# Kernel optimization log

Measured on AMD Instinct MI355X. Metric: run time of the kernel, lower is better.

The kernel has to match this reference:

```python
import jax, jax.numpy as jnp
import numpy as np

EPS = 0.07      # sinkhorn temperature
ITERS = 7       # sinkhorn iterations
TINY = 1e-8
NORM_EPS = 1e-12  # F.normalize default clamp


def setup_inputs() -> dict:
    key = jax.random.key(0)
    k1, k2 = jax.random.split(key)
    x = jax.random.normal(k1, (64, 2048, 24, 12), dtype=jnp.float32)
    anchors = jax.random.normal(k2, (2, 2048), dtype=jnp.float32) * 0.02
    return {"x": x, "anchors": anchors}


def reference(x, anchors):
    B, C, H, W = x.shape
    HW = H * W
    # tokens: (B, HW, C)
    X = x.reshape(B, C, HW).transpose(0, 2, 1)
    Xn = X / jnp.maximum(jnp.linalg.norm(X, axis=-1, keepdims=True), NORM_EPS)
    An = anchors / jnp.maximum(jnp.linalg.norm(anchors, axis=-1, keepdims=True), NORM_EPS)
    # cosine cost (B, HW, 2)
    Cmat = 1.0 - jnp.einsum('bhc,kc->bhk', Xn, An)
    Kmat = jnp.exp(-Cmat / max(EPS, TINY)) + TINY
    a = jnp.full((B, HW), 1.0 / HW, dtype=Kmat.dtype)
    b = jnp.full((B, 2), 0.5, dtype=Kmat.dtype)

    def step(carry, _):
        u, v = carry
        Kv = jnp.einsum('bhk,bk->bh', Kmat, v) + TINY
        u = a / Kv
        KTu = jnp.einsum('bhk,bh->bk', Kmat, u) + TINY
        v = b / KTu
        return (u, v), None

    u0 = jnp.ones((B, HW), dtype=Kmat.dtype)
    v0 = jnp.ones((B, 2), dtype=Kmat.dtype)
    (u, v), _ = jax.lax.scan(step, (u0, v0), None, length=ITERS)
    # transport plan and soft masks
    P = Kmat * u[:, :, None] * v[:, None, :]          # (B, HW, 2)
    m = (P * HW).transpose(0, 2, 1).reshape(B, 2, H, W)
    # masked pooling for both prototypes at once
    num = jnp.einsum('bchw,bkhw->bkc', x, m)           # (B, 2, C)
    den = m.sum(axis=(2, 3)) + 1e-6                    # (B, 2)
    c = num / den[:, :, None]
    c0_vec = c[:, 0][:, :, None, None]                 # (B, C, 1, 1)
    c1_vec = c[:, 1][:, :, None, None]
    return (c0_vec, c1_vec, m)
```

## Files before the change

### kernel.cpp

```cpp
#include <hip/hip_runtime.h>

#define B_    64
#define C_    2048
#define HW_   288
#define EPS_  0.07f
#define TINY_ 1e-8f

__device__ __forceinline__ void acc3(const float4 v, float a0, float a1,
                                     float* ssq, float* sd0, float* sd1) {
  ssq[0] += v.x * v.x; ssq[1] += v.y * v.y; ssq[2] += v.z * v.z; ssq[3] += v.w * v.w;
  sd0[0] += v.x * a0;  sd0[1] += v.y * a0;  sd0[2] += v.z * a0;  sd0[3] += v.w * a0;
  sd1[0] += v.x * a1;  sd1[1] += v.y * a1;  sd1[2] += v.z * a1;  sd1[3] += v.w * a1;
}

__global__ __launch_bounds__(256) void k1_partials(
    const float* __restrict__ x, const float* __restrict__ anchors,
    float* __restrict__ part, int nch, int cpc) {
  int bi = blockIdx.x;
  int nblk = nch >> 2;
  int b  = bi / nblk;
  int cg = bi - b * nblk;
  int t = threadIdx.x, lane = t & 63, wid = t >> 6;
  int ch = cg * 4 + wid;
  int c0 = ch * cpc;
  const float* xb = x + ((size_t)b * C_ + c0) * HW_;
  bool tail = lane < 8;

  float ssq[4] = {0,0,0,0}, sd0[4] = {0,0,0,0}, sd1[4] = {0,0,0,0};
  float tsq[4] = {0,0,0,0}, td0[4] = {0,0,0,0}, td1[4] = {0,0,0,0};

#pragma unroll 4
  for (int r = 0; r < cpc; ++r) {
    const float4* xr = (const float4*)(xb + (size_t)r * HW_);
    float a0 = anchors[c0 + r];
    float a1 = anchors[C_ + c0 + r];
    float4 xa = xr[lane];
    acc3(xa, a0, a1, ssq, sd0, sd1);
    if (tail) {
      float4 xc = xr[64 + lane];
      acc3(xc, a0, a1, tsq, td0, td1);
    }
  }

  size_t PS = (size_t)B_ * nch * HW_;
  float* base = part + (size_t)(b * nch + ch) * HW_;
  float4* p0 = (float4*)base;
  float4* p1 = (float4*)(base + PS);
  float4* p2 = (float4*)(base + 2 * PS);
  p0[lane] = make_float4(ssq[0], ssq[1], ssq[2], ssq[3]);
  p1[lane] = make_float4(sd0[0], sd0[1], sd0[2], sd0[3]);
  p2[lane] = make_float4(sd1[0], sd1[1], sd1[2], sd1[3]);
  if (tail) {
    p0[64 + lane] = make_float4(tsq[0], tsq[1], tsq[2], tsq[3]);
    p1[64 + lane] = make_float4(td0[0], td0[1], td0[2], td0[3]);
    p2[64 + lane] = make_float4(td1[0], td1[1], td1[2], td1[3]);
  }
}

__global__ __launch_bounds__(256) void k1b_reduce(
    const float* __restrict__ part, float* __restrict__ red, int nch) {
  int idx = blockIdx.x * 256 + threadIdx.x;
  int plane = idx / (B_ * HW_);
  int rem = idx - plane * (B_ * HW_);
  int b = rem / HW_;
  int h = rem - b * HW_;
  const float* p = part + (size_t)plane * B_ * nch * HW_ + (size_t)b * nch * HW_ + h;
  float s = 0.f;
#pragma unroll 8
  for (int ch = 0; ch < nch; ++ch) s += p[(size_t)ch * HW_];
  red[idx] = s;
}

__device__ __forceinline__ void block_reduce2(
    float& p0, float& p1, volatile float* red0, volatile float* red1,
    int t, int nw) {
  int lane = t & 63, wid = t >> 6;
#pragma unroll
  for (int off = 32; off >= 1; off >>= 1) {
    p0 += __shfl_down(p0, off);
    p1 += __shfl_down(p1, off);
  }
  __syncthreads();
  if (lane == 0) { red0[wid] = p0; red1[wid] = p1; }
  __syncthreads();
  float s0 = 0.f, s1 = 0.f;
  for (int w = 0; w < nw; ++w) { s0 += red0[w]; s1 += red1[w]; }
  p0 = s0; p1 = s1;
}

__global__ __launch_bounds__(320) void k2_sinkhorn(
    const float* __restrict__ red, const float* __restrict__ anchors,
    float* __restrict__ out_m, float* __restrict__ invden) {
  int b = blockIdx.x, t = threadIdx.x;
  __shared__ float red0[8], red1[8];
  const int nw = 5;

  float a0 = 0.f, a1 = 0.f;
  for (int c = t; c < C_; c += 320) {
    float q0 = anchors[c], q1 = anchors[C_ + c];
    a0 += q0 * q0; a1 += q1 * q1;
  }
  block_reduce2(a0, a1, red0, red1, t, nw);
  float ian0 = 1.0f / fmaxf(sqrtf(a0), 1e-12f);
  float ian1 = 1.0f / fmaxf(sqrtf(a1), 1e-12f);

  float K0 = 0.f, K1 = 0.f;
  if (t < HW_) {
    float ssq = red[b * HW_ + t];
    float d0  = red[B_ * HW_ + b * HW_ + t];
    float d1  = red[2 * B_ * HW_ + b * HW_ + t];
    float ixn = 1.0f / fmaxf(sqrtf(ssq), 1e-12f);
    float cos0 = d0 * ixn * ian0;
    float cos1 = d1 * ixn * ian1;
    K0 = expf((cos0 - 1.0f) / EPS_) + TINY_;
    K1 = expf((cos1 - 1.0f) / EPS_) + TINY_;
  }

  float v0 = 1.f, v1 = 1.f, u = 0.f;
  for (int it = 0; it < 7; ++it) {
    if (t < HW_) u = (1.0f / (float)HW_) / (K0 * v0 + K1 * v1 + TINY_);
    float p0 = K0 * u, p1 = K1 * u;
    block_reduce2(p0, p1, red0, red1, t, nw);
    v0 = 0.5f / (p0 + TINY_);
    v1 = 0.5f / (p1 + TINY_);
  }

  float m0 = 0.f, m1 = 0.f;
  if (t < HW_) {
    m0 = K0 * u * v0 * (float)HW_;
    m1 = K1 * u * v1 * (float)HW_;
  }
  float q0 = m0, q1 = m1;
  block_reduce2(q0, q1, red0, red1, t, nw);
  if (t < HW_) {
    out_m[(b * 2 + 0) * HW_ + t] = m0;
    out_m[(b * 2 + 1) * HW_ + t] = m1;
  }
  if (t == 0) {
    invden[b * 2 + 0] = 1.0f / (q0 + 1e-6f);
    invden[b * 2 + 1] = 1.0f / (q1 + 1e-6f);
  }
}

__global__ __launch_bounds__(256) void k3_pool(
    const float* __restrict__ x, const float* __restrict__ m,
    const float* __restrict__ invden, float* __restrict__ out) {
  int bi = blockIdx.x;
  int b = bi >> 4, seg = bi & 15;
  int t = threadIdx.x;
  int lr = t >> 1, half = t & 1;
  int c = seg * 128 + lr;

  __shared__ float4 sm0[72], sm1[72];
  __shared__ float sinv[2];
  if (t < 72)       sm0[t]      = ((const float4*)(m + (b * 2 + 0) * HW_))[t];
  else if (t < 144) sm1[t - 72] = ((const float4*)(m + (b * 2 + 1) * HW_))[t - 72];
  if (t == 0) { sinv[0] = invden[2 * b]; sinv[1] = invden[2 * b + 1]; }
  __syncthreads();

  const float4* xr = (const float4*)(x + ((size_t)b * C_ + c) * HW_) + half * 36;
  const float4* w0p = sm0 + half * 36;
  const float4* w1p = sm1 + half * 36;
  float acc0 = 0.f, acc1 = 0.f;
#pragma unroll 4
  for (int i = 0; i < 36; ++i) {
    float4 xa = xr[i];
    float4 w0 = w0p[i];
    float4 w1 = w1p[i];
    acc0 += xa.x * w0.x + xa.y * w0.y + xa.z * w0.z + xa.w * w0.w;
    acc1 += xa.x * w1.x + xa.y * w1.y + xa.z * w1.z + xa.w * w1.w;
  }
  acc0 += __shfl_down(acc0, 1);
  acc1 += __shfl_down(acc1, 1);
  if (half == 0) {
    out[(size_t)b * C_ + c] = acc0 * sinv[0];
    out[(size_t)B_ * C_ + (size_t)b * C_ + c] = acc1 * sinv[1];
  }
}

extern "C" void kernel_launch(void* const* d_in, const int* in_sizes, int n_in,
                              void* d_out, int out_size, void* d_ws, size_t ws_size,
                              hipStream_t stream) {
  const float* x       = (const float*)d_in[0];
  const float* anchors = (const float*)d_in[1];
  float* out = (float*)d_out;

  float* invden = (float*)d_ws;
  float* red = invden + 128;
  float* part = red + 3 * B_ * HW_;
  int nch = 128;
  while (nch > 4 &&
         (size_t)(128 + 3 * B_ * HW_ + 3 * B_ * nch * HW_) * sizeof(float) > ws_size)
    nch >>= 1;
  int cpc = C_ / nch;

  float* out_m = out + 2 * B_ * C_;

  k1_partials<<<B_ * (nch / 4), 256, 0, stream>>>(x, anchors, part, nch, cpc);
  k1b_reduce<<<(3 * B_ * HW_) / 256, 256, 0, stream>>>(part, red, nch);
  k2_sinkhorn<<<B_, 320, 0, stream>>>(red, anchors, out_m, invden);
  k3_pool<<<B_ * 16, 256, 0, stream>>>(x, out_m, invden, out);
}
```

Before: 266.2 us.

## Restructure pooling kernel with register-held masks and fewer k1 channel splits

The pooling kernel now has 8 threads cooperate on each channel row, each reading a contiguous 9-float4 slice. Each thread keeps its mask weights in registers instead of shared memory, and each block loops over 256 channels. This gives coalesced row reads and removes the shared-memory staging and barrier, at the cost of 72 extra registers per thread and fewer blocks. Separately, the k1 channel split drops from 128 to 32, which shrinks the partial-sum buffer and the reduce pass. The trade-off is less parallelism in the first pass over x.

```diff
diff --git a/kernel.cpp b/kernel.cpp
--- a/kernel.cpp
+++ b/kernel.cpp
@@ -146,35 +146,40 @@
     const float* __restrict__ x, const float* __restrict__ m,
     const float* __restrict__ invden, float* __restrict__ out) {
   int bi = blockIdx.x;
-  int b = bi >> 4, seg = bi & 15;
-  int t = threadIdx.x;
-  int lr = t >> 1, half = t & 1;
-  int c = seg * 128 + lr;
-
-  __shared__ float4 sm0[72], sm1[72];
-  __shared__ float sinv[2];
-  if (t < 72)       sm0[t]      = ((const float4*)(m + (b * 2 + 0) * HW_))[t];
-  else if (t < 144) sm1[t - 72] = ((const float4*)(m + (b * 2 + 1) * HW_))[t - 72];
-  if (t == 0) { sinv[0] = invden[2 * b]; sinv[1] = invden[2 * b + 1]; }
-  __syncthreads();
-
-  const float4* xr = (const float4*)(x + ((size_t)b * C_ + c) * HW_) + half * 36;
-  const float4* w0p = sm0 + half * 36;
-  const float4* w1p = sm1 + half * 36;
-  float acc0 = 0.f, acc1 = 0.f;
-#pragma unroll 4
-  for (int i = 0; i < 36; ++i) {
-    float4 xa = xr[i];
-    float4 w0 = w0p[i];
-    float4 w1 = w1p[i];
-    acc0 += xa.x * w0.x + xa.y * w0.y + xa.z * w0.z + xa.w * w0.w;
-    acc1 += xa.x * w1.x + xa.y * w1.y + xa.z * w1.z + xa.w * w1.w;
-  }
-  acc0 += __shfl_down(acc0, 1);
-  acc1 += __shfl_down(acc1, 1);
-  if (half == 0) {
-    out[(size_t)b * C_ + c] = acc0 * sinv[0];
-    out[(size_t)B_ * C_ + (size_t)b * C_ + c] = acc1 * sinv[1];
+  int b = bi >> 3, seg = bi & 7;
+  int t = threadIdx.x, oct = t & 7, rl = t >> 3;
+
+  const float4* m0 = (const float4*)(m + (b * 2 + 0) * HW_);
+  const float4* m1 = (const float4*)(m + (b * 2 + 1) * HW_);
+  float4 w0[9], w1[9];
+#pragma unroll
+  for (int j = 0; j < 9; ++j) {
+    w0[j] = m0[oct * 9 + j];
+    w1[j] = m1[oct * 9 + j];
+  }
+  float inv0 = invden[2 * b], inv1 = invden[2 * b + 1];
+
+  int cbase = seg * 256;
+#pragma unroll 2
+  for (int g = 0; g < 8; ++g) {
+    int c = cbase + g * 32 + rl;
+    const float4* xr = (const float4*)(x + ((size_t)b * C_ + c) * HW_) + oct * 9;
+    float a0 = 0.f, a1 = 0.f;
+#pragma unroll
+    for (int j = 0; j < 9; ++j) {
+      float4 xa = xr[j];
+      a0 += xa.x * w0[j].x + xa.y * w0[j].y + xa.z * w0[j].z + xa.w * w0[j].w;
+      a1 += xa.x * w1[j].x + xa.y * w1[j].y + xa.z * w1[j].z + xa.w * w1[j].w;
+    }
+#pragma unroll
+    for (int off = 4; off >= 1; off >>= 1) {
+      a0 += __shfl_xor(a0, off);
+      a1 += __shfl_xor(a1, off);
+    }
+    if (oct == 0) {
+      out[(size_t)b * C_ + c] = a0 * inv0;
+      out[(size_t)B_ * C_ + (size_t)b * C_ + c] = a1 * inv1;
+    }
   }
 }
 
@@ -188,7 +193,7 @@
   float* invden = (float*)d_ws;
   float* red = invden + 128;
   float* part = red + 3 * B_ * HW_;
-  int nch = 128;
+  int nch = 32;
   while (nch > 4 &&
          (size_t)(128 + 3 * B_ * HW_ + 3 * B_ * nch * HW_) * sizeof(float) > ws_size)
     nch >>= 1;
@@ -199,5 +204,5 @@
   k1_partials<<<B_ * (nch / 4), 256, 0, stream>>>(x, anchors, part, nch, cpc);
   k1b_reduce<<<(3 * B_ * HW_) / 256, 256, 0, stream>>>(part, red, nch);
   k2_sinkhorn<<<B_, 320, 0, stream>>>(red, anchors, out_m, invden);
-  k3_pool<<<B_ * 16, 256, 0, stream>>>(x, out_m, invden, out);
-}
+  k3_pool<<<B_ * 8, 256, 0, stream>>>(x, out_m, invden, out);
+}
```

Measured after the change: 276.5 us. +3.9%, slower.
